# Performance work log

Hardware: AMD Instinct MI355X
Metric: run time of the kernel (lower is better)

## Reference

```python
import jax, jax.numpy as jnp
import numpy as np

N = 100000
E = 1000000
IN, HID, OUT = 128, 64, 40


def setup_inputs() -> dict:
    key = jax.random.key(0)
    k1, k2, k3, k4 = jax.random.split(key, 4)
    x = jax.random.normal(k1, (N, IN), dtype=jnp.float32)
    edge_index = jax.random.randint(k2, (2, E), 0, N, dtype=jnp.int64)
    W1 = jax.random.normal(k3, (IN, HID), dtype=jnp.float32) * (1.0 / np.sqrt(IN))
    b1 = jnp.zeros((HID,), dtype=jnp.float32)
    W2 = jax.random.normal(k4, (HID, OUT), dtype=jnp.float32) * (1.0 / np.sqrt(HID))
    b2 = jnp.zeros((OUT,), dtype=jnp.float32)
    return {"x": x, "edge_index": edge_index, "W1": W1, "b1": b1, "W2": W2, "b2": b2}


def _gcn_norm(edge_index, num_nodes):
    # PyG GCNConv default: add self-loops, symmetric normalization deg^-1/2 A deg^-1/2
    loop = jnp.arange(num_nodes, dtype=edge_index.dtype)
    src = jnp.concatenate([edge_index[0], loop])
    dst = jnp.concatenate([edge_index[1], loop])
    deg = jax.ops.segment_sum(jnp.ones_like(dst, dtype=jnp.float32), dst, num_segments=num_nodes)
    dinv = jnp.where(deg > 0, jax.lax.rsqrt(deg), 0.0)
    norm = dinv[src] * dinv[dst]  # [E+N]
    return src, dst, norm


def _gcn_conv(h, W, b, src, dst, norm, num_nodes):
    h = h @ W                          # [N, d_out] dense transform
    msg = h[src] * norm[:, None]       # gather + scale per edge
    out = jax.ops.segment_sum(msg, dst, num_segments=num_nodes)  # scatter-add
    return out + b


def reference(x, edge_index, W1, b1, W2, b2):
    src, dst, norm = _gcn_norm(edge_index, N)
    h = jax.nn.relu(_gcn_conv(x, W1, b1, src, dst, norm, N))
    # dropout is identity at inference (module in eval mode)
    out = _gcn_conv(h, W2, b2, src, dst, norm, N)
    return out
```

## Files before the change

### kernel.cpp

```cpp
#include <hip/hip_runtime.h>

#define NN 100000
#define EE 1000000
#define IN_F 128
#define HID_F 64
#define OUT_F 40
#define BUCKET 48
#define BIN_NODES 256
#define NBINS 391
#define FIFO_CAP 4096
#define P1_CHUNK 2048
#define P1_BUF 16

typedef _Float16 half8 __attribute__((ext_vector_type(8)));
typedef _Float16 half4 __attribute__((ext_vector_type(4)));
typedef float f32x4 __attribute__((ext_vector_type(4)));

#define SWZ(b, row) ((b) ^ (((row) & 7) << 4))

static __device__ __forceinline__ int atomic_add_i32(int* p, int v) {
    return __hip_atomic_fetch_add(p, v, __ATOMIC_RELAXED, __HIP_MEMORY_SCOPE_AGENT);
}

static __device__ __forceinline__ f32x4 h4f4(half4 h) {
    f32x4 r = {(float)h.x, (float)h.y, (float)h.z, (float)h.w};
    return r;
}

__global__ __launch_bounds__(256) void k_prep(const float* __restrict__ W1,
                                              const float* __restrict__ W2,
                                              _Float16* __restrict__ w1t,
                                              _Float16* __restrict__ w2t,
                                              int* __restrict__ bincur) {
    int i = blockIdx.x * 256 + threadIdx.x;
    if (i < IN_F * HID_F) {
        int k = i >> 6, n = i & 63;
        w1t[n * IN_F + k] = (_Float16)W1[i];
    }
    if (i < 48 * HID_F) {
        int n = i >> 6, k = i & 63;
        w2t[i] = (_Float16)((n < OUT_F) ? W2[k * OUT_F + n] : 0.f);
    }
    if (i < NBINS) bincur[i] = 0;
}

__global__ __launch_bounds__(256) void k_bin(const int* __restrict__ ei,
                                             int* __restrict__ bincur,
                                             unsigned* __restrict__ fifo) {
    __shared__ unsigned buf[NBINS][P1_BUF];
    __shared__ int lcnt[NBINS];
    __shared__ int lbase[NBINS];
    const int tid = threadIdx.x;
    for (int j = tid; j < NBINS; j += 256) lcnt[j] = 0;
    __syncthreads();

    const int e0 = blockIdx.x * P1_CHUNK;
    #pragma unroll
    for (int i = 0; i < P1_CHUNK / 256; ++i) {
        int e = e0 + i * 256 + tid;
        if (e < EE) {
            int s = ei[e];
            int d = ei[EE + e];
            int bin = d >> 8;
            unsigned pk = ((unsigned)s << 8) | (unsigned)(d & 255);
            int p = atomicAdd(&lcnt[bin], 1);
            if (p < P1_BUF) {
                buf[bin][p] = pk;
            } else {
                int gp = atomic_add_i32(&bincur[bin], 1);
                if (gp < FIFO_CAP) fifo[(size_t)bin * FIFO_CAP + gp] = pk;
            }
        }
    }
    __syncthreads();
    for (int j = tid; j < NBINS; j += 256) {
        int cnt = lcnt[j]; if (cnt > P1_BUF) cnt = P1_BUF;
        lbase[j] = (cnt > 0) ? atomic_add_i32(&bincur[j], cnt) : 0;
        lcnt[j] = cnt;
    }
    __syncthreads();
    for (int j = tid; j < NBINS; j += 256) {
        int cnt = lcnt[j];
        int base = lbase[j];
        for (int k = 0; k < cnt; ++k) {
            int gp = base + k;
            if (gp < FIFO_CAP) fifo[(size_t)j * FIFO_CAP + gp] = buf[j][k];
        }
    }
}

__global__ __launch_bounds__(256) void k_csr(const int* __restrict__ bincur,
                                             const unsigned* __restrict__ fifo,
                                             int* __restrict__ csr,
                                             int* __restrict__ deg,
                                             float* __restrict__ dinv) {
    __shared__ int cur[BIN_NODES];
    __shared__ int stage[BIN_NODES * BUCKET];
    const int tid = threadIdx.x;
    const int bin = blockIdx.x;
    const int v0 = bin * BIN_NODES;
    const int nnode = (NN - v0 < BIN_NODES) ? (NN - v0) : BIN_NODES;
    if (tid < BIN_NODES) cur[tid] = 0;
    __syncthreads();

    int cnt = bincur[bin]; if (cnt > FIFO_CAP) cnt = FIFO_CAP;
    for (int k = tid; k < cnt; k += 256) {
        unsigned u = fifo[(size_t)bin * FIFO_CAP + k];
        int dl = u & 255;
        int s = (int)(u >> 8);
        int p = atomicAdd(&cur[dl], 1);
        if (p < BUCKET) stage[dl * BUCKET + p] = s;
    }
    __syncthreads();

    if (tid < nnode) {
        int d = cur[tid]; if (d > BUCKET) d = BUCKET;
        int dpad = (d + 7) & ~7; if (dpad > BUCKET) dpad = BUCKET;
        for (int k = d; k < dpad; ++k) stage[tid * BUCKET + k] = NN;
        cur[tid] = d;
    }
    __syncthreads();

    const int total4 = nnode * BUCKET / 4;
    int4* dst4 = (int4*)&csr[(size_t)v0 * BUCKET];
    for (int idx = tid; idx < total4; idx += 256)
        dst4[idx] = *(const int4*)&stage[idx * 4];
    if (tid < nnode) {
        int d = cur[tid];
        deg[v0 + tid] = d;
        dinv[v0 + tid] = rsqrtf((float)(d + 1));
    }
}

__global__ __launch_bounds__(256) void k_gemm1(const float* __restrict__ x,
                                               const _Float16* __restrict__ w1t,
                                               const float* __restrict__ dinv,
                                               _Float16* __restrict__ h1s) {
    __shared__ _Float16 As[64 * IN_F];
    __shared__ _Float16 Bs[64 * IN_F];
    const int tid = threadIdx.x;
    const size_t r0 = (size_t)blockIdx.x * 64;

    #pragma unroll
    for (int i = 0; i < 8; ++i) {
        int f = i * 256 + tid;
        int row = f >> 5;
        int k4 = (f & 31) * 4;
        size_t gr = r0 + row; if (gr >= NN) gr = NN - 1;
        float4 v = *(const float4*)&x[gr * IN_F + k4];
        _Float16 h[4] = {(_Float16)v.x, (_Float16)v.y, (_Float16)v.z, (_Float16)v.w};
        *(uint2*)((char*)As + SWZ(row * 256 + k4 * 2, row)) = *(uint2*)h;
    }
    #pragma unroll
    for (int i = 0; i < 4; ++i) {
        int c = i * 256 + tid;
        int col = c >> 4;
        int k8 = (c & 15) * 8;
        uint4 v = *(const uint4*)&w1t[col * IN_F + k8];
        *(uint4*)((char*)Bs + SWZ(col * 256 + k8 * 2, col)) = v;
    }
    __syncthreads();

    const int w = tid >> 6, l = tid & 63;
    const int lr = l & 15, lg = l >> 4;
    const int R0 = w * 16;
    f32x4 acc[4] = {};
    #pragma unroll
    for (int kk = 0; kk < 4; ++kk) {
        const int kbyte = (kk * 32 + lg * 8) * 2;
        const int arow = R0 + lr;
        half8 a = *(const half8*)((const char*)As + SWZ(arow * 256 + kbyte, arow));
        #pragma unroll
        for (int t = 0; t < 4; ++t) {
            const int bcol = t * 16 + lr;
            half8 b = *(const half8*)((const char*)Bs + SWZ(bcol * 256 + kbyte, bcol));
            acc[t] = __builtin_amdgcn_mfma_f32_16x16x32_f16(a, b, acc[t], 0, 0, 0);
        }
    }
    #pragma unroll
    for (int r = 0; r < 4; ++r) {
        size_t row = r0 + R0 + lg * 4 + r;
        if (row < NN) {
            float dv = dinv[row];
            #pragma unroll
            for (int t = 0; t < 4; ++t)
                h1s[row * HID_F + t * 16 + lr] = (_Float16)(dv * acc[t][r]);
        } else if (row == NN) {
            #pragma unroll
            for (int t = 0; t < 4; ++t)
                h1s[row * HID_F + t * 16 + lr] = (_Float16)0.f;
        }
    }
}

__global__ __launch_bounds__(256) void k_agg1g2(const _Float16* __restrict__ h1s,
                                                const float* __restrict__ dinv,
                                                const int* __restrict__ degA,
                                                const int* __restrict__ csr,
                                                const float* __restrict__ b1,
                                                const _Float16* __restrict__ w2t,
                                                _Float16* __restrict__ tabA,
                                                _Float16* __restrict__ tabB) {
    __shared__ _Float16 As[64 * HID_F];
    __shared__ _Float16 Bs[48 * HID_F];
    const int tid = threadIdx.x;
    const size_t r0 = (size_t)blockIdx.x * 64;

    for (int cB = tid; cB < 384; cB += 256) {
        int col = cB >> 3;
        int k8 = (cB & 7) * 8;
        uint4 vB = *(const uint4*)&w2t[col * HID_F + k8];
        *(uint4*)((char*)Bs + SWZ(col * 128 + k8 * 2, col)) = vB;
    }

    const int grp = tid >> 4;
    const int c = tid & 15;
    float4 bb = *(const float4*)&b1[c * 4];
    #pragma unroll
    for (int i = 0; i < 4; ++i) {
        const int row = grp + i * 16;
        const size_t v = r0 + row;
        if (v >= NN) continue;

        int dg = degA[v];
        if (dg > BUCKET) dg = BUCKET;
        const int iters = (dg + 7) >> 3;
        const int4* cp = (const int4*)&csr[(size_t)v * BUCKET];

        f32x4 accA = h4f4(*(const half4*)&h1s[(v << 6) + c * 4]);
        f32x4 accB = {};
        for (int it = 0; it < iters; ++it) {
            int4 sa = cp[2 * it];
            int4 sb = cp[2 * it + 1];
            half4 a0 = *(const half4*)&h1s[((size_t)sa.x << 6) + c * 4];
            half4 a1 = *(const half4*)&h1s[((size_t)sa.y << 6) + c * 4];
            half4 a2 = *(const half4*)&h1s[((size_t)sa.z << 6) + c * 4];
            half4 a3 = *(const half4*)&h1s[((size_t)sa.w << 6) + c * 4];
            half4 a4 = *(const half4*)&h1s[((size_t)sb.x << 6) + c * 4];
            half4 a5 = *(const half4*)&h1s[((size_t)sb.y << 6) + c * 4];
            half4 a6 = *(const half4*)&h1s[((size_t)sb.z << 6) + c * 4];
            half4 a7 = *(const half4*)&h1s[((size_t)sb.w << 6) + c * 4];
            accA += h4f4(a0); accB += h4f4(a1); accA += h4f4(a2); accB += h4f4(a3);
            accA += h4f4(a4); accB += h4f4(a5); accA += h4f4(a6); accB += h4f4(a7);
        }
        accA += accB;

        const float dv = dinv[v];
        _Float16 o[4];
        o[0] = (_Float16)fmaxf(dv * accA[0] + bb.x, 0.f);
        o[1] = (_Float16)fmaxf(dv * accA[1] + bb.y, 0.f);
        o[2] = (_Float16)fmaxf(dv * accA[2] + bb.z, 0.f);
        o[3] = (_Float16)fmaxf(dv * accA[3] + bb.w, 0.f);
        *(uint2*)((char*)As + SWZ(row * 128 + c * 8, row)) = *(uint2*)o;
    }
    __syncthreads();

    const int w = tid >> 6, l = tid & 63;
    const int lr = l & 15, lg = l >> 4;
    const int R0 = w * 16;
    f32x4 acc[3] = {};
    #pragma unroll
    for (int kk = 0; kk < 2; ++kk) {
        const int kbyte = (kk * 32 + lg * 8) * 2;
        const int arow = R0 + lr;
        half8 a = *(const half8*)((const char*)As + SWZ(arow * 128 + kbyte, arow));
        #pragma unroll
        for (int t = 0; t < 3; ++t) {
            const int bcol = t * 16 + lr;
            half8 b = *(const half8*)((const char*)Bs + SWZ(bcol * 128 + kbyte, bcol));
            acc[t] = __builtin_amdgcn_mfma_f32_16x16x32_f16(a, b, acc[t], 0, 0, 0);
        }
    }
    #pragma unroll
    for (int r = 0; r < 4; ++r) {
        size_t row = r0 + R0 + lg * 4 + r;
        if (row < NN) {
            float dv = dinv[row];
            #pragma unroll
            for (int t = 0; t < 3; ++t) {
                int col = t * 16 + lr;
                float val = dv * acc[t][r];
                if (col < 32) tabA[row * 32 + col] = (_Float16)val;
                else if (col < OUT_F) tabB[row * 8 + (col - 32)] = (_Float16)val;
            }
        } else if (row == NN) {
            #pragma unroll
            for (int t = 0; t < 3; ++t) {
                int col = t * 16 + lr;
                if (col < 32) tabA[row * 32 + col] = (_Float16)0.f;
                else if (col < OUT_F) tabB[row * 8 + (col - 32)] = (_Float16)0.f;
            }
        }
    }
}

__global__ __launch_bounds__(256) void k_agg2(const _Float16* __restrict__ tabA,
                                              const _Float16* __restrict__ tabB,
                                              const float* __restrict__ dinv,
                                              const int* __restrict__ degA,
                                              const int* __restrict__ csr,
                                              const float* __restrict__ b2,
                                              float* __restrict__ out) {
    const int tid = threadIdx.x;
    const int v = blockIdx.x * 16 + (tid >> 4);
    if (v >= NN) return;
    const int c = tid & 15;
    const bool useA = (c < 8);
    const size_t aoff = useA ? (size_t)c * 4 : 0;
    const size_t boff = (c >= 8 && c < 10) ? (size_t)(c - 8) * 4 : 0;

    int dg = degA[v];
    if (dg > BUCKET) dg = BUCKET;
    const int iters = (dg + 7) >> 3;
    const int4* cp = (const int4*)&csr[(size_t)v * BUCKET];

    f32x4 accA, accB = {};
    {
        const _Float16* p = useA ? tabA + ((size_t)v << 5) + aoff : tabB + ((size_t)v << 3) + boff;
        accA = h4f4(*(const half4*)p);
    }
    for (int it = 0; it < iters; ++it) {
        int4 sa = cp[2 * it];
        int4 sb = cp[2 * it + 1];
        const _Float16* p0 = useA ? tabA + ((size_t)sa.x << 5) + aoff : tabB + ((size_t)sa.x << 3) + boff;
        const _Float16* p1 = useA ? tabA + ((size_t)sa.y << 5) + aoff : tabB + ((size_t)sa.y << 3) + boff;
        const _Float16* p2 = useA ? tabA + ((size_t)sa.z << 5) + aoff : tabB + ((size_t)sa.z << 3) + boff;
        const _Float16* p3 = useA ? tabA + ((size_t)sa.w << 5) + aoff : tabB + ((size_t)sa.w << 3) + boff;
        const _Float16* p4 = useA ? tabA + ((size_t)sb.x << 5) + aoff : tabB + ((size_t)sb.x << 3) + boff;
        const _Float16* p5 = useA ? tabA + ((size_t)sb.y << 5) + aoff : tabB + ((size_t)sb.y << 3) + boff;
        const _Float16* p6 = useA ? tabA + ((size_t)sb.z << 5) + aoff : tabB + ((size_t)sb.z << 3) + boff;
        const _Float16* p7 = useA ? tabA + ((size_t)sb.w << 5) + aoff : tabB + ((size_t)sb.w << 3) + boff;
        half4 a0 = *(const half4*)p0;
        half4 a1 = *(const half4*)p1;
        half4 a2 = *(const half4*)p2;
        half4 a3 = *(const half4*)p3;
        half4 a4 = *(const half4*)p4;
        half4 a5 = *(const half4*)p5;
        half4 a6 = *(const half4*)p6;
        half4 a7 = *(const half4*)p7;
        accA += h4f4(a0); accB += h4f4(a1); accA += h4f4(a2); accB += h4f4(a3);
        accA += h4f4(a4); accB += h4f4(a5); accA += h4f4(a6); accB += h4f4(a7);
    }
    accA += accB;

    if (c < 10) {
        const float dv = dinv[v];
        float4 bb = *(const float4*)&b2[c * 4];
        float4 o = {dv * accA[0] + bb.x, dv * accA[1] + bb.y,
                    dv * accA[2] + bb.z, dv * accA[3] + bb.w};
        *(float4*)&out[(size_t)v * OUT_F + c * 4] = o;
    }
}

extern "C" void kernel_launch(void* const* d_in, const int* in_sizes, int n_in,
                              void* d_out, int out_size, void* d_ws, size_t ws_size,
                              hipStream_t stream) {
    const float* x  = (const float*)d_in[0];
    const int*   ei = (const int*)d_in[1];
    const float* W1 = (const float*)d_in[2];
    const float* b1 = (const float*)d_in[3];
    const float* W2 = (const float*)d_in[4];
    const float* b2 = (const float*)d_in[5];
    float* out = (float*)d_out;

    char* p = (char*)d_ws;
    float*     dinv   = (float*)p;     p += (size_t)NN * 4;
    int*       deg    = (int*)p;       p += (size_t)NN * 4;
    int*       bincur = (int*)p;       p += 512 * 4;
    unsigned*  fifo   = (unsigned*)p;  p += (size_t)NBINS * FIFO_CAP * 4;
    _Float16*  w1t    = (_Float16*)p;  p += (size_t)IN_F * HID_F * 2;
    _Float16*  w2t    = (_Float16*)p;  p += (size_t)48 * HID_F * 2;
    int*       csr    = (int*)p;       p += (size_t)NN * BUCKET * 4;
    _Float16*  h1s    = (_Float16*)p;  p += (size_t)(NN + 1) * HID_F * 2;
    _Float16*  tabA   = (_Float16*)p;  p += (size_t)(NN + 1) * 32 * 2;
    _Float16*  tabB   = (_Float16*)p;  p += ((size_t)(NN + 1) * 8 + 32) * 2;

    const int gemm_blocks = (NN + 63) / 64;
    const int agg2_blocks = (NN + 15) / 16;
    const int bin_blocks = (EE + P1_CHUNK - 1) / P1_CHUNK;

    k_prep  <<<32, 256, 0, stream>>>(W1, W2, w1t, w2t, bincur);
    k_bin   <<<bin_blocks, 256, 0, stream>>>(ei, bincur, fifo);
    k_csr   <<<NBINS, 256, 0, stream>>>(bincur, fifo, csr, deg, dinv);
    k_gemm1 <<<gemm_blocks, 256, 0, stream>>>(x, w1t, dinv, h1s);
    k_agg1g2<<<gemm_blocks, 256, 0, stream>>>(h1s, dinv, deg, csr, b1, w2t, tabA, tabB);
    k_agg2  <<<agg2_blocks, 256, 0, stream>>>(tabA, tabB, dinv, deg, csr, b2, out);
}
```

Before: 106.2 us.

## Merge edge binning with first GEMM in one launch; apply source dinv during aggregation

The edge-binning pass and the dense X·W1 transform now run as separate block ranges of a single kernel, so the two independent stages can overlap on the GPU. To make that possible, the GEMM no longer scales rows by dinv, because dinv is only computed later in the CSR kernel. The aggregation kernel therefore gathers dinv per source edge, and each block converts W1 and W2 to fp16 itself instead of using a prep kernel. The bincur reset becomes a memset. The cost is an extra dinv gather per edge in aggregation and a slower, strided W1 transpose repeated in every GEMM block.

```diff
diff --git a/kernel.cpp b/kernel.cpp
--- a/kernel.cpp
+++ b/kernel.cpp
@@ -11,6 +11,8 @@
 #define FIFO_CAP 4096
 #define P1_CHUNK 2048
 #define P1_BUF 16
+#define BIN_BLOCKS ((EE + P1_CHUNK - 1) / P1_CHUNK)
+#define GEMM_BLOCKS ((NN + 63) / 64)
 
 typedef _Float16 half8 __attribute__((ext_vector_type(8)));
 typedef _Float16 half4 __attribute__((ext_vector_type(4)));
@@ -27,64 +29,105 @@
     return r;
 }
 
-__global__ __launch_bounds__(256) void k_prep(const float* __restrict__ W1,
-                                              const float* __restrict__ W2,
-                                              _Float16* __restrict__ w1t,
-                                              _Float16* __restrict__ w2t,
-                                              int* __restrict__ bincur) {
-    int i = blockIdx.x * 256 + threadIdx.x;
-    if (i < IN_F * HID_F) {
-        int k = i >> 6, n = i & 63;
-        w1t[n * IN_F + k] = (_Float16)W1[i];
-    }
-    if (i < 48 * HID_F) {
-        int n = i >> 6, k = i & 63;
-        w2t[i] = (_Float16)((n < OUT_F) ? W2[k * OUT_F + n] : 0.f);
-    }
-    if (i < NBINS) bincur[i] = 0;
-}
-
-__global__ __launch_bounds__(256) void k_bin(const int* __restrict__ ei,
+__global__ __launch_bounds__(256) void k_fat(const int* __restrict__ ei,
                                              int* __restrict__ bincur,
-                                             unsigned* __restrict__ fifo) {
-    __shared__ unsigned buf[NBINS][P1_BUF];
-    __shared__ int lcnt[NBINS];
-    __shared__ int lbase[NBINS];
+                                             unsigned* __restrict__ fifo,
+                                             const float* __restrict__ x,
+                                             const float* __restrict__ W1,
+                                             _Float16* __restrict__ h1) {
+    __shared__ __align__(16) char smem[32768];
     const int tid = threadIdx.x;
-    for (int j = tid; j < NBINS; j += 256) lcnt[j] = 0;
-    __syncthreads();
-
-    const int e0 = blockIdx.x * P1_CHUNK;
-    #pragma unroll
-    for (int i = 0; i < P1_CHUNK / 256; ++i) {
-        int e = e0 + i * 256 + tid;
-        if (e < EE) {
-            int s = ei[e];
-            int d = ei[EE + e];
-            int bin = d >> 8;
-            unsigned pk = ((unsigned)s << 8) | (unsigned)(d & 255);
-            int p = atomicAdd(&lcnt[bin], 1);
-            if (p < P1_BUF) {
-                buf[bin][p] = pk;
-            } else {
-                int gp = atomic_add_i32(&bincur[bin], 1);
-                if (gp < FIFO_CAP) fifo[(size_t)bin * FIFO_CAP + gp] = pk;
-            }
-        }
-    }
-    __syncthreads();
-    for (int j = tid; j < NBINS; j += 256) {
-        int cnt = lcnt[j]; if (cnt > P1_BUF) cnt = P1_BUF;
-        lbase[j] = (cnt > 0) ? atomic_add_i32(&bincur[j], cnt) : 0;
-        lcnt[j] = cnt;
-    }
-    __syncthreads();
-    for (int j = tid; j < NBINS; j += 256) {
-        int cnt = lcnt[j];
-        int base = lbase[j];
-        for (int k = 0; k < cnt; ++k) {
-            int gp = base + k;
-            if (gp < FIFO_CAP) fifo[(size_t)j * FIFO_CAP + gp] = buf[j][k];
+
+    if (blockIdx.x < BIN_BLOCKS) {
+        unsigned (*buf)[P1_BUF] = (unsigned (*)[P1_BUF])smem;
+        int* lcnt  = (int*)(smem + 25024);
+        int* lbase = (int*)(smem + 25024 + 1600);
+        for (int j = tid; j < NBINS; j += 256) lcnt[j] = 0;
+        __syncthreads();
+
+        const int e0 = blockIdx.x * P1_CHUNK;
+        #pragma unroll
+        for (int i = 0; i < P1_CHUNK / 256; ++i) {
+            int e = e0 + i * 256 + tid;
+            if (e < EE) {
+                int s = ei[e];
+                int d = ei[EE + e];
+                int bin = d >> 8;
+                unsigned pk = ((unsigned)s << 8) | (unsigned)(d & 255);
+                int p = atomicAdd(&lcnt[bin], 1);
+                if (p < P1_BUF) {
+                    buf[bin][p] = pk;
+                } else {
+                    int gp = atomic_add_i32(&bincur[bin], 1);
+                    if (gp < FIFO_CAP) fifo[(size_t)bin * FIFO_CAP + gp] = pk;
+                }
+            }
+        }
+        __syncthreads();
+        for (int j = tid; j < NBINS; j += 256) {
+            int cnt = lcnt[j]; if (cnt > P1_BUF) cnt = P1_BUF;
+            lbase[j] = (cnt > 0) ? atomic_add_i32(&bincur[j], cnt) : 0;
+            lcnt[j] = cnt;
+        }
+        __syncthreads();
+        for (int j = tid; j < NBINS; j += 256) {
+            int cnt = lcnt[j];
+            int base = lbase[j];
+            for (int k = 0; k < cnt; ++k) {
+                int gp = base + k;
+                if (gp < FIFO_CAP) fifo[(size_t)j * FIFO_CAP + gp] = buf[j][k];
+            }
+        }
+    } else {
+        _Float16* As = (_Float16*)smem;
+        _Float16* Bs = (_Float16*)(smem + 16384);
+        const size_t r0 = (size_t)(blockIdx.x - BIN_BLOCKS) * 64;
+
+        #pragma unroll
+        for (int i = 0; i < 8; ++i) {
+            int f = i * 256 + tid;
+            int row = f >> 5;
+            int k4 = (f & 31) * 4;
+            size_t gr = r0 + row; if (gr >= NN) gr = NN - 1;
+            float4 v = *(const float4*)&x[gr * IN_F + k4];
+            _Float16 h[4] = {(_Float16)v.x, (_Float16)v.y, (_Float16)v.z, (_Float16)v.w};
+            *(uint2*)((char*)As + SWZ(row * 256 + k4 * 2, row)) = *(uint2*)h;
+        }
+        for (int i = tid; i < IN_F * HID_F; i += 256) {
+            int col = i >> 7, k = i & 127;
+            _Float16 w = (_Float16)W1[k * HID_F + col];
+            *(_Float16*)((char*)Bs + SWZ(col * 256 + k * 2, col)) = w;
+        }
+        __syncthreads();
+
+        const int w = tid >> 6, l = tid & 63;
+        const int lr = l & 15, lg = l >> 4;
+        const int R0 = w * 16;
+        f32x4 acc[4] = {};
+        #pragma unroll
+        for (int kk = 0; kk < 4; ++kk) {
+            const int kbyte = (kk * 32 + lg * 8) * 2;
+            const int arow = R0 + lr;
+            half8 a = *(const half8*)((const char*)As + SWZ(arow * 256 + kbyte, arow));
+            #pragma unroll
+            for (int t = 0; t < 4; ++t) {
+                const int bcol = t * 16 + lr;
+                half8 b = *(const half8*)((const char*)Bs + SWZ(bcol * 256 + kbyte, bcol));
+                acc[t] = __builtin_amdgcn_mfma_f32_16x16x32_f16(a, b, acc[t], 0, 0, 0);
+            }
+        }
+        #pragma unroll
+        for (int r = 0; r < 4; ++r) {
+            size_t row = r0 + R0 + lg * 4 + r;
+            if (row < NN) {
+                #pragma unroll
+                for (int t = 0; t < 4; ++t)
+                    h1[row * HID_F + t * 16 + lr] = (_Float16)acc[t][r];
+            } else if (row == NN) {
+                #pragma unroll
+                for (int t = 0; t < 4; ++t)
+                    h1[row * HID_F + t * 16 + lr] = (_Float16)0.f;
+            }
         }
     }
 }
@@ -130,75 +173,15 @@
         deg[v0 + tid] = d;
         dinv[v0 + tid] = rsqrtf((float)(d + 1));
     }
-}
-
-__global__ __launch_bounds__(256) void k_gemm1(const float* __restrict__ x,
-                                               const _Float16* __restrict__ w1t,
-                                               const float* __restrict__ dinv,
-                                               _Float16* __restrict__ h1s) {
-    __shared__ _Float16 As[64 * IN_F];
-    __shared__ _Float16 Bs[64 * IN_F];
-    const int tid = threadIdx.x;
-    const size_t r0 = (size_t)blockIdx.x * 64;
-
-    #pragma unroll
-    for (int i = 0; i < 8; ++i) {
-        int f = i * 256 + tid;
-        int row = f >> 5;
-        int k4 = (f & 31) * 4;
-        size_t gr = r0 + row; if (gr >= NN) gr = NN - 1;
-        float4 v = *(const float4*)&x[gr * IN_F + k4];
-        _Float16 h[4] = {(_Float16)v.x, (_Float16)v.y, (_Float16)v.z, (_Float16)v.w};
-        *(uint2*)((char*)As + SWZ(row * 256 + k4 * 2, row)) = *(uint2*)h;
-    }
-    #pragma unroll
-    for (int i = 0; i < 4; ++i) {
-        int c = i * 256 + tid;
-        int col = c >> 4;
-        int k8 = (c & 15) * 8;
-        uint4 v = *(const uint4*)&w1t[col * IN_F + k8];
-        *(uint4*)((char*)Bs + SWZ(col * 256 + k8 * 2, col)) = v;
-    }
-    __syncthreads();
-
-    const int w = tid >> 6, l = tid & 63;
-    const int lr = l & 15, lg = l >> 4;
-    const int R0 = w * 16;
-    f32x4 acc[4] = {};
-    #pragma unroll
-    for (int kk = 0; kk < 4; ++kk) {
-        const int kbyte = (kk * 32 + lg * 8) * 2;
-        const int arow = R0 + lr;
-        half8 a = *(const half8*)((const char*)As + SWZ(arow * 256 + kbyte, arow));
-        #pragma unroll
-        for (int t = 0; t < 4; ++t) {
-            const int bcol = t * 16 + lr;
-            half8 b = *(const half8*)((const char*)Bs + SWZ(bcol * 256 + kbyte, bcol));
-            acc[t] = __builtin_amdgcn_mfma_f32_16x16x32_f16(a, b, acc[t], 0, 0, 0);
-        }
-    }
-    #pragma unroll
-    for (int r = 0; r < 4; ++r) {
-        size_t row = r0 + R0 + lg * 4 + r;
-        if (row < NN) {
-            float dv = dinv[row];
-            #pragma unroll
-            for (int t = 0; t < 4; ++t)
-                h1s[row * HID_F + t * 16 + lr] = (_Float16)(dv * acc[t][r]);
-        } else if (row == NN) {
-            #pragma unroll
-            for (int t = 0; t < 4; ++t)
-                h1s[row * HID_F + t * 16 + lr] = (_Float16)0.f;
-        }
-    }
-}
-
-__global__ __launch_bounds__(256) void k_agg1g2(const _Float16* __restrict__ h1s,
+    if (bin == 0 && tid == 0) dinv[NN] = 0.f;
+}
+
+__global__ __launch_bounds__(256) void k_agg1g2(const _Float16* __restrict__ h1,
                                                 const float* __restrict__ dinv,
                                                 const int* __restrict__ degA,
                                                 const int* __restrict__ csr,
                                                 const float* __restrict__ b1,
-                                                const _Float16* __restrict__ w2t,
+                                                const float* __restrict__ W2,
                                                 _Float16* __restrict__ tabA,
                                                 _Float16* __restrict__ tabB) {
     __shared__ _Float16 As[64 * HID_F];
@@ -206,11 +189,10 @@
     const int tid = threadIdx.x;
     const size_t r0 = (size_t)blockIdx.x * 64;
 
-    for (int cB = tid; cB < 384; cB += 256) {
-        int col = cB >> 3;
-        int k8 = (cB & 7) * 8;
-        uint4 vB = *(const uint4*)&w2t[col * HID_F + k8];
-        *(uint4*)((char*)Bs + SWZ(col * 128 + k8 * 2, col)) = vB;
+    for (int i = tid; i < 48 * HID_F; i += 256) {
+        int col = i >> 6, k = i & 63;
+        _Float16 w = (_Float16)((col < OUT_F) ? W2[k * OUT_F + col] : 0.f);
+        *(_Float16*)((char*)Bs + SWZ(col * 128 + k * 2, col)) = w;
     }
 
     const int grp = tid >> 4;
@@ -227,30 +209,34 @@
         const int iters = (dg + 7) >> 3;
         const int4* cp = (const int4*)&csr[(size_t)v * BUCKET];
 
-        f32x4 accA = h4f4(*(const half4*)&h1s[(v << 6) + c * 4]);
+        const float dvv = dinv[v];
+        f32x4 accA = dvv * h4f4(*(const half4*)&h1[(v << 6) + c * 4]);
         f32x4 accB = {};
         for (int it = 0; it < iters; ++it) {
             int4 sa = cp[2 * it];
             int4 sb = cp[2 * it + 1];
-            half4 a0 = *(const half4*)&h1s[((size_t)sa.x << 6) + c * 4];
-            half4 a1 = *(const half4*)&h1s[((size_t)sa.y << 6) + c * 4];
-            half4 a2 = *(const half4*)&h1s[((size_t)sa.z << 6) + c * 4];
-            half4 a3 = *(const half4*)&h1s[((size_t)sa.w << 6) + c * 4];
-            half4 a4 = *(const half4*)&h1s[((size_t)sb.x << 6) + c * 4];
-            half4 a5 = *(const half4*)&h1s[((size_t)sb.y << 6) + c * 4];
-            half4 a6 = *(const half4*)&h1s[((size_t)sb.z << 6) + c * 4];
-            half4 a7 = *(const half4*)&h1s[((size_t)sb.w << 6) + c * 4];
-            accA += h4f4(a0); accB += h4f4(a1); accA += h4f4(a2); accB += h4f4(a3);
-            accA += h4f4(a4); accB += h4f4(a5); accA += h4f4(a6); accB += h4f4(a7);
+            float d0 = dinv[sa.x], d1 = dinv[sa.y], d2 = dinv[sa.z], d3 = dinv[sa.w];
+            float d4 = dinv[sb.x], d5 = dinv[sb.y], d6 = dinv[sb.z], d7 = dinv[sb.w];
+            half4 a0 = *(const half4*)&h1[((size_t)sa.x << 6) + c * 4];
+            half4 a1 = *(const half4*)&h1[((size_t)sa.y << 6) + c * 4];
+            half4 a2 = *(const half4*)&h1[((size_t)sa.z << 6) + c * 4];
+            half4 a3 = *(const half4*)&h1[((size_t)sa.w << 6) + c * 4];
+            half4 a4 = *(const half4*)&h1[((size_t)sb.x << 6) + c * 4];
+            half4 a5 = *(const half4*)&h1[((size_t)sb.y << 6) + c * 4];
+            half4 a6 = *(const half4*)&h1[((size_t)sb.z << 6) + c * 4];
+            half4 a7 = *(const half4*)&h1[((size_t)sb.w << 6) + c * 4];
+            accA += d0 * h4f4(a0); accB += d1 * h4f4(a1);
+            accA += d2 * h4f4(a2); accB += d3 * h4f4(a3);
+            accA += d4 * h4f4(a4); accB += d5 * h4f4(a5);
+            accA += d6 * h4f4(a6); accB += d7 * h4f4(a7);
         }
         accA += accB;
 
-        const float dv = dinv[v];
         _Float16 o[4];
-        o[0] = (_Float16)fmaxf(dv * accA[0] + bb.x, 0.f);
-        o[1] = (_Float16)fmaxf(dv * accA[1] + bb.y, 0.f);
-        o[2] = (_Float16)fmaxf(dv * accA[2] + bb.z, 0.f);
-        o[3] = (_Float16)fmaxf(dv * accA[3] + bb.w, 0.f);
+        o[0] = (_Float16)fmaxf(dvv * accA[0] + bb.x, 0.f);
+        o[1] = (_Float16)fmaxf(dvv * accA[1] + bb.y, 0.f);
+        o[2] = (_Float16)fmaxf(dvv * accA[2] + bb.z, 0.f);
+        o[3] = (_Float16)fmaxf(dvv * accA[3] + bb.w, 0.f);
         *(uint2*)((char*)As + SWZ(row * 128 + c * 8, row)) = *(uint2*)o;
     }
     __syncthreads();
@@ -364,25 +350,20 @@
     float* out = (float*)d_out;
 
     char* p = (char*)d_ws;
-    float*     dinv   = (float*)p;     p += (size_t)NN * 4;
+    float*     dinv   = (float*)p;     p += (size_t)(NN + 1) * 4;
     int*       deg    = (int*)p;       p += (size_t)NN * 4;
     int*       bincur = (int*)p;       p += 512 * 4;
     unsigned*  fifo   = (unsigned*)p;  p += (size_t)NBINS * FIFO_CAP * 4;
-    _Float16*  w1t    = (_Float16*)p;  p += (size_t)IN_F * HID_F * 2;
-    _Float16*  w2t    = (_Float16*)p;  p += (size_t)48 * HID_F * 2;
     int*       csr    = (int*)p;       p += (size_t)NN * BUCKET * 4;
-    _Float16*  h1s    = (_Float16*)p;  p += (size_t)(NN + 1) * HID_F * 2;
+    _Float16*  h1     = (_Float16*)p;  p += (size_t)(NN + 1) * HID_F * 2;
     _Float16*  tabA   = (_Float16*)p;  p += (size_t)(NN + 1) * 32 * 2;
     _Float16*  tabB   = (_Float16*)p;  p += ((size_t)(NN + 1) * 8 + 32) * 2;
 
-    const int gemm_blocks = (NN + 63) / 64;
     const int agg2_blocks = (NN + 15) / 16;
-    const int bin_blocks = (EE + P1_CHUNK - 1) / P1_CHUNK;
-
-    k_prep  <<<32, 256, 0, stream>>>(W1, W2, w1t, w2t, bincur);
-    k_bin   <<<bin_blocks, 256, 0, stream>>>(ei, bincur, fifo);
+
+    hipMemsetAsync(bincur, 0, 512 * 4, stream);
+    k_fat   <<<BIN_BLOCKS + GEMM_BLOCKS, 256, 0, stream>>>(ei, bincur, fifo, x, W1, h1);
     k_csr   <<<NBINS, 256, 0, stream>>>(bincur, fifo, csr, deg, dinv);
-    k_gemm1 <<<gemm_blocks, 256, 0, stream>>>(x, w1t, dinv, h1s);
-    k_agg1g2<<<gemm_blocks, 256, 0, stream>>>(h1s, dinv, deg, csr, b1, w2t, tabA, tabB);
+    k_agg1g2<<<GEMM_BLOCKS, 256, 0, stream>>>(h1, dinv, deg, csr, b1, W2, tabA, tabB);
     k_agg2  <<<agg2_blocks, 256, 0, stream>>>(tabA, tabB, dinv, deg, csr, b2, out);
 }
```

Result: slower. 159.9 us (+50.6%).

## Replace global bin FIFO atomics with per-block fixed segments plus small overflow

Applied to the files above, without the earlier changes.

The edge binning pass now writes each block's per-bin local buffer into a fixed, private segment indexed by (bin, block), with a per-segment count, and drops the per-bin global atomic reservation. Only edges that overflow the 16-entry local buffer go through a global atomic into a small per-bin overflow FIFO. The CSR builder walks each bin's per-block segments and then the overflow list. This removes global atomic contention in the binning pass, but the CSR kernel now reads segments serially per thread, and the overflow capacity of 64 per bin may silently drop edges if a block's local buffer overflows often.

```diff
diff --git a/kernel.cpp b/kernel.cpp
--- a/kernel.cpp
+++ b/kernel.cpp
@@ -8,9 +8,10 @@
 #define BUCKET 48
 #define BIN_NODES 256
 #define NBINS 391
-#define FIFO_CAP 4096
 #define P1_CHUNK 2048
 #define P1_BUF 16
+#define BIN_BLOCKS ((EE + P1_CHUNK - 1) / P1_CHUNK)
+#define OV_CAP 64
 
 typedef _Float16 half8 __attribute__((ext_vector_type(8)));
 typedef _Float16 half4 __attribute__((ext_vector_type(4)));
@@ -31,7 +32,7 @@
                                               const float* __restrict__ W2,
                                               _Float16* __restrict__ w1t,
                                               _Float16* __restrict__ w2t,
-                                              int* __restrict__ bincur) {
+                                              int* __restrict__ ocnt) {
     int i = blockIdx.x * 256 + threadIdx.x;
     if (i < IN_F * HID_F) {
         int k = i >> 6, n = i & 63;
@@ -41,20 +42,22 @@
         int n = i >> 6, k = i & 63;
         w2t[i] = (_Float16)((n < OUT_F) ? W2[k * OUT_F + n] : 0.f);
     }
-    if (i < NBINS) bincur[i] = 0;
+    if (i < NBINS) ocnt[i] = 0;
 }
 
 __global__ __launch_bounds__(256) void k_bin(const int* __restrict__ ei,
-                                             int* __restrict__ bincur,
-                                             unsigned* __restrict__ fifo) {
+                                             int* __restrict__ ocnt,
+                                             unsigned* __restrict__ ofifo,
+                                             int* __restrict__ lcnt2,
+                                             unsigned* __restrict__ fifo2) {
     __shared__ unsigned buf[NBINS][P1_BUF];
     __shared__ int lcnt[NBINS];
-    __shared__ int lbase[NBINS];
-    const int tid = threadIdx.x;
+    const int tid = threadIdx.x;
+    const int b = blockIdx.x;
     for (int j = tid; j < NBINS; j += 256) lcnt[j] = 0;
     __syncthreads();
 
-    const int e0 = blockIdx.x * P1_CHUNK;
+    const int e0 = b * P1_CHUNK;
     #pragma unroll
     for (int i = 0; i < P1_CHUNK / 256; ++i) {
         int e = e0 + i * 256 + tid;
@@ -67,30 +70,24 @@
             if (p < P1_BUF) {
                 buf[bin][p] = pk;
             } else {
-                int gp = atomic_add_i32(&bincur[bin], 1);
-                if (gp < FIFO_CAP) fifo[(size_t)bin * FIFO_CAP + gp] = pk;
+                int gp = atomic_add_i32(&ocnt[bin], 1);
+                if (gp < OV_CAP) ofifo[bin * OV_CAP + gp] = pk;
             }
         }
     }
     __syncthreads();
     for (int j = tid; j < NBINS; j += 256) {
         int cnt = lcnt[j]; if (cnt > P1_BUF) cnt = P1_BUF;
-        lbase[j] = (cnt > 0) ? atomic_add_i32(&bincur[j], cnt) : 0;
-        lcnt[j] = cnt;
-    }
-    __syncthreads();
-    for (int j = tid; j < NBINS; j += 256) {
-        int cnt = lcnt[j];
-        int base = lbase[j];
-        for (int k = 0; k < cnt; ++k) {
-            int gp = base + k;
-            if (gp < FIFO_CAP) fifo[(size_t)j * FIFO_CAP + gp] = buf[j][k];
-        }
-    }
-}
-
-__global__ __launch_bounds__(256) void k_csr(const int* __restrict__ bincur,
-                                             const unsigned* __restrict__ fifo,
+        lcnt2[j * BIN_BLOCKS + b] = cnt;
+        unsigned* seg = &fifo2[((size_t)j * BIN_BLOCKS + b) * P1_BUF];
+        for (int k = 0; k < cnt; ++k) seg[k] = buf[j][k];
+    }
+}
+
+__global__ __launch_bounds__(256) void k_csr(const int* __restrict__ lcnt2,
+                                             const unsigned* __restrict__ fifo2,
+                                             const int* __restrict__ ocnt,
+                                             const unsigned* __restrict__ ofifo,
                                              int* __restrict__ csr,
                                              int* __restrict__ deg,
                                              float* __restrict__ dinv) {
@@ -103,13 +100,26 @@
     if (tid < BIN_NODES) cur[tid] = 0;
     __syncthreads();
 
-    int cnt = bincur[bin]; if (cnt > FIFO_CAP) cnt = FIFO_CAP;
-    for (int k = tid; k < cnt; k += 256) {
-        unsigned u = fifo[(size_t)bin * FIFO_CAP + k];
-        int dl = u & 255;
-        int s = (int)(u >> 8);
-        int p = atomicAdd(&cur[dl], 1);
-        if (p < BUCKET) stage[dl * BUCKET + p] = s;
+    for (int blk = tid; blk < BIN_BLOCKS; blk += 256) {
+        int cnt = lcnt2[bin * BIN_BLOCKS + blk];
+        const unsigned* seg = &fifo2[((size_t)bin * BIN_BLOCKS + blk) * P1_BUF];
+        for (int k = 0; k < cnt; ++k) {
+            unsigned u = seg[k];
+            int dl = u & 255;
+            int s = (int)(u >> 8);
+            int p = atomicAdd(&cur[dl], 1);
+            if (p < BUCKET) stage[dl * BUCKET + p] = s;
+        }
+    }
+    {
+        int oc = ocnt[bin]; if (oc > OV_CAP) oc = OV_CAP;
+        for (int k = tid; k < oc; k += 256) {
+            unsigned u = ofifo[bin * OV_CAP + k];
+            int dl = u & 255;
+            int s = (int)(u >> 8);
+            int p = atomicAdd(&cur[dl], 1);
+            if (p < BUCKET) stage[dl * BUCKET + p] = s;
+        }
     }
     __syncthreads();
 
@@ -366,8 +376,10 @@
     char* p = (char*)d_ws;
     float*     dinv   = (float*)p;     p += (size_t)NN * 4;
     int*       deg    = (int*)p;       p += (size_t)NN * 4;
-    int*       bincur = (int*)p;       p += 512 * 4;
-    unsigned*  fifo   = (unsigned*)p;  p += (size_t)NBINS * FIFO_CAP * 4;
+    int*       ocnt   = (int*)p;       p += 512 * 4;
+    unsigned*  ofifo  = (unsigned*)p;  p += (size_t)NBINS * OV_CAP * 4;
+    int*       lcnt2  = (int*)p;       p += (size_t)NBINS * BIN_BLOCKS * 4;
+    unsigned*  fifo2  = (unsigned*)p;  p += (size_t)NBINS * BIN_BLOCKS * P1_BUF * 4;
     _Float16*  w1t    = (_Float16*)p;  p += (size_t)IN_F * HID_F * 2;
     _Float16*  w2t    = (_Float16*)p;  p += (size_t)48 * HID_F * 2;
     int*       csr    = (int*)p;       p += (size_t)NN * BUCKET * 4;
@@ -377,11 +389,10 @@
 
     const int gemm_blocks = (NN + 63) / 64;
     const int agg2_blocks = (NN + 15) / 16;
-    const int bin_blocks = (EE + P1_CHUNK - 1) / P1_CHUNK;
-
-    k_prep  <<<32, 256, 0, stream>>>(W1, W2, w1t, w2t, bincur);
-    k_bin   <<<bin_blocks, 256, 0, stream>>>(ei, bincur, fifo);
-    k_csr   <<<NBINS, 256, 0, stream>>>(bincur, fifo, csr, deg, dinv);
+
+    k_prep  <<<32, 256, 0, stream>>>(W1, W2, w1t, w2t, ocnt);
+    k_bin   <<<BIN_BLOCKS, 256, 0, stream>>>(ei, ocnt, ofifo, lcnt2, fifo2);
+    k_csr   <<<NBINS, 256, 0, stream>>>(lcnt2, fifo2, ocnt, ofifo, csr, deg, dinv);
     k_gemm1 <<<gemm_blocks, 256, 0, stream>>>(x, w1t, dinv, h1s);
     k_agg1g2<<<gemm_blocks, 256, 0, stream>>>(h1s, dinv, deg, csr, b1, w2t, tabA, tabB);
     k_agg2  <<<agg2_blocks, 256, 0, stream>>>(tabA, tabB, dinv, deg, csr, b2, out);
```

New measurement: 116.7 us. 1.1x slower.

## Slice feature tables into 16-column planes for cache-local gather aggregation

Applied to the files above, without the earlier changes.

Stores the hidden and output feature tables as separate 16-column planes (32 bytes per node). Block indices are interleaved so that concurrently running blocks work on the same plane and its working set can stay in L2/MALL during the random neighbor gathers. This splits the fused aggregate+GEMM2 kernel into a separate aggregation kernel and a GEMM2 kernel, which adds a kernel launch and a round trip of the ReLU activations through global memory. The output gather is also padded to 48 columns across three planes.

```diff
diff --git a/kernel.cpp b/kernel.cpp
--- a/kernel.cpp
+++ b/kernel.cpp
@@ -11,6 +11,7 @@
 #define FIFO_CAP 4096
 #define P1_CHUNK 2048
 #define P1_BUF 16
+#define NWORK 1563
 
 typedef _Float16 half8 __attribute__((ext_vector_type(8)));
 typedef _Float16 half4 __attribute__((ext_vector_type(4)));
@@ -135,7 +136,7 @@
 __global__ __launch_bounds__(256) void k_gemm1(const float* __restrict__ x,
                                                const _Float16* __restrict__ w1t,
                                                const float* __restrict__ dinv,
-                                               _Float16* __restrict__ h1s) {
+                                               _Float16* __restrict__ h1sl) {
     __shared__ _Float16 As[64 * IN_F];
     __shared__ _Float16 Bs[64 * IN_F];
     const int tid = threadIdx.x;
@@ -184,74 +185,88 @@
             float dv = dinv[row];
             #pragma unroll
             for (int t = 0; t < 4; ++t)
-                h1s[row * HID_F + t * 16 + lr] = (_Float16)(dv * acc[t][r]);
+                h1sl[((size_t)t * (NN + 1) + row) * 16 + lr] = (_Float16)(dv * acc[t][r]);
         } else if (row == NN) {
             #pragma unroll
             for (int t = 0; t < 4; ++t)
-                h1s[row * HID_F + t * 16 + lr] = (_Float16)0.f;
-        }
-    }
-}
-
-__global__ __launch_bounds__(256) void k_agg1g2(const _Float16* __restrict__ h1s,
+                h1sl[((size_t)t * (NN + 1) + row) * 16 + lr] = (_Float16)0.f;
+        }
+    }
+}
+
+__global__ __launch_bounds__(256) void k_agg1sl(const _Float16* __restrict__ h1sl,
                                                 const float* __restrict__ dinv,
-                                                const int* __restrict__ degA,
+                                                const int* __restrict__ deg,
                                                 const int* __restrict__ csr,
                                                 const float* __restrict__ b1,
-                                                const _Float16* __restrict__ w2t,
-                                                _Float16* __restrict__ tabA,
-                                                _Float16* __restrict__ tabB) {
+                                                _Float16* __restrict__ hrelusl) {
+    const int b = blockIdx.x;
+    const int s = (b & 7) >> 1;
+    const int w = ((b >> 3) << 1) | (b & 1);
+    if (w >= NWORK) return;
+    const int tid = threadIdx.x;
+    const int v = w * 64 + (tid >> 2);
+    if (v >= NN) return;
+    const int c = tid & 3;
+
+    const _Float16* tab = h1sl + (size_t)s * (NN + 1) * 16;
+    int dg = deg[v];
+    if (dg > BUCKET) dg = BUCKET;
+    const int iters = (dg + 7) >> 3;
+    const int4* cp = (const int4*)&csr[(size_t)v * BUCKET];
+
+    f32x4 accA = h4f4(*(const half4*)&tab[(size_t)v * 16 + c * 4]);
+    f32x4 accB = {};
+    for (int it = 0; it < iters; ++it) {
+        int4 sa = cp[2 * it];
+        int4 sb = cp[2 * it + 1];
+        half4 a0 = *(const half4*)&tab[(size_t)sa.x * 16 + c * 4];
+        half4 a1 = *(const half4*)&tab[(size_t)sa.y * 16 + c * 4];
+        half4 a2 = *(const half4*)&tab[(size_t)sa.z * 16 + c * 4];
+        half4 a3 = *(const half4*)&tab[(size_t)sa.w * 16 + c * 4];
+        half4 a4 = *(const half4*)&tab[(size_t)sb.x * 16 + c * 4];
+        half4 a5 = *(const half4*)&tab[(size_t)sb.y * 16 + c * 4];
+        half4 a6 = *(const half4*)&tab[(size_t)sb.z * 16 + c * 4];
+        half4 a7 = *(const half4*)&tab[(size_t)sb.w * 16 + c * 4];
+        accA += h4f4(a0); accB += h4f4(a1); accA += h4f4(a2); accB += h4f4(a3);
+        accA += h4f4(a4); accB += h4f4(a5); accA += h4f4(a6); accB += h4f4(a7);
+    }
+    accA += accB;
+
+    const float dv = dinv[v];
+    float4 bb = *(const float4*)&b1[s * 16 + c * 4];
+    _Float16 o[4];
+    o[0] = (_Float16)fmaxf(dv * accA[0] + bb.x, 0.f);
+    o[1] = (_Float16)fmaxf(dv * accA[1] + bb.y, 0.f);
+    o[2] = (_Float16)fmaxf(dv * accA[2] + bb.z, 0.f);
+    o[3] = (_Float16)fmaxf(dv * accA[3] + bb.w, 0.f);
+    *(uint2*)&hrelusl[((size_t)s * (NN + 1) + v) * 16 + c * 4] = *(uint2*)o;
+}
+
+__global__ __launch_bounds__(256) void k_gemm2(const _Float16* __restrict__ hrelusl,
+                                               const _Float16* __restrict__ w2t,
+                                               const float* __restrict__ dinv,
+                                               _Float16* __restrict__ tabsl) {
     __shared__ _Float16 As[64 * HID_F];
     __shared__ _Float16 Bs[48 * HID_F];
     const int tid = threadIdx.x;
     const size_t r0 = (size_t)blockIdx.x * 64;
 
+    #pragma unroll
+    for (int i = 0; i < 2; ++i) {
+        int cI = i * 256 + tid;
+        int row = cI >> 3;
+        int sc = cI & 7;
+        size_t gr = r0 + row; if (gr >= NN) gr = NN - 1;
+        const _Float16* src = hrelusl + ((size_t)(sc >> 1) * (NN + 1) + gr) * 16 + (sc & 1) * 8;
+        uint4 v = *(const uint4*)src;
+        *(uint4*)((char*)As + SWZ(row * 128 + sc * 16, row)) = v;
+    }
     for (int cB = tid; cB < 384; cB += 256) {
         int col = cB >> 3;
         int k8 = (cB & 7) * 8;
         uint4 vB = *(const uint4*)&w2t[col * HID_F + k8];
         *(uint4*)((char*)Bs + SWZ(col * 128 + k8 * 2, col)) = vB;
-    }
-
-    const int grp = tid >> 4;
-    const int c = tid & 15;
-    float4 bb = *(const float4*)&b1[c * 4];
-    #pragma unroll
-    for (int i = 0; i < 4; ++i) {
-        const int row = grp + i * 16;
-        const size_t v = r0 + row;
-        if (v >= NN) continue;
-
-        int dg = degA[v];
-        if (dg > BUCKET) dg = BUCKET;
-        const int iters = (dg + 7) >> 3;
-        const int4* cp = (const int4*)&csr[(size_t)v * BUCKET];
-
-        f32x4 accA = h4f4(*(const half4*)&h1s[(v << 6) + c * 4]);
-        f32x4 accB = {};
-        for (int it = 0; it < iters; ++it) {
-            int4 sa = cp[2 * it];
-            int4 sb = cp[2 * it + 1];
-            half4 a0 = *(const half4*)&h1s[((size_t)sa.x << 6) + c * 4];
-            half4 a1 = *(const half4*)&h1s[((size_t)sa.y << 6) + c * 4];
-            half4 a2 = *(const half4*)&h1s[((size_t)sa.z << 6) + c * 4];
-            half4 a3 = *(const half4*)&h1s[((size_t)sa.w << 6) + c * 4];
-            half4 a4 = *(const half4*)&h1s[((size_t)sb.x << 6) + c * 4];
-            half4 a5 = *(const half4*)&h1s[((size_t)sb.y << 6) + c * 4];
-            half4 a6 = *(const half4*)&h1s[((size_t)sb.z << 6) + c * 4];
-            half4 a7 = *(const half4*)&h1s[((size_t)sb.w << 6) + c * 4];
-            accA += h4f4(a0); accB += h4f4(a1); accA += h4f4(a2); accB += h4f4(a3);
-            accA += h4f4(a4); accB += h4f4(a5); accA += h4f4(a6); accB += h4f4(a7);
-        }
-        accA += accB;
-
-        const float dv = dinv[v];
-        _Float16 o[4];
-        o[0] = (_Float16)fmaxf(dv * accA[0] + bb.x, 0.f);
-        o[1] = (_Float16)fmaxf(dv * accA[1] + bb.y, 0.f);
-        o[2] = (_Float16)fmaxf(dv * accA[2] + bb.z, 0.f);
-        o[3] = (_Float16)fmaxf(dv * accA[3] + bb.w, 0.f);
-        *(uint2*)((char*)As + SWZ(row * 128 + c * 8, row)) = *(uint2*)o;
     }
     __syncthreads();
 
@@ -279,76 +294,68 @@
             #pragma unroll
             for (int t = 0; t < 3; ++t) {
                 int col = t * 16 + lr;
-                float val = dv * acc[t][r];
-                if (col < 32) tabA[row * 32 + col] = (_Float16)val;
-                else if (col < OUT_F) tabB[row * 8 + (col - 32)] = (_Float16)val;
+                float val = (col < OUT_F) ? dv * acc[t][r] : 0.f;
+                tabsl[((size_t)t * (NN + 1) + row) * 16 + lr] = (_Float16)val;
             }
         } else if (row == NN) {
             #pragma unroll
-            for (int t = 0; t < 3; ++t) {
-                int col = t * 16 + lr;
-                if (col < 32) tabA[row * 32 + col] = (_Float16)0.f;
-                else if (col < OUT_F) tabB[row * 8 + (col - 32)] = (_Float16)0.f;
-            }
-        }
-    }
-}
-
-__global__ __launch_bounds__(256) void k_agg2(const _Float16* __restrict__ tabA,
-                                              const _Float16* __restrict__ tabB,
-                                              const float* __restrict__ dinv,
-                                              const int* __restrict__ degA,
-                                              const int* __restrict__ csr,
-                                              const float* __restrict__ b2,
-                                              float* __restrict__ out) {
-    const int tid = threadIdx.x;
-    const int v = blockIdx.x * 16 + (tid >> 4);
+            for (int t = 0; t < 3; ++t)
+                tabsl[((size_t)t * (NN + 1) + row) * 16 + lr] = (_Float16)0.f;
+        }
+    }
+}
+
+__global__ __launch_bounds__(256) void k_agg2sl(const _Float16* __restrict__ tabsl,
+                                                const float* __restrict__ dinv,
+                                                const int* __restrict__ deg,
+                                                const int* __restrict__ csr,
+                                                const float* __restrict__ b2,
+                                                float* __restrict__ out) {
+    const int b = blockIdx.x;
+    const int m = b & 7;
+    int s, i3, per;
+    if (m < 3)      { s = 0; i3 = m;     per = 3; }
+    else if (m < 6) { s = 1; i3 = m - 3; per = 3; }
+    else            { s = 2; i3 = m - 6; per = 2; }
+    const int w = (b >> 3) * per + i3;
+    if (w >= NWORK) return;
+    const int tid = threadIdx.x;
+    const int c = tid & 3;
+    if (s == 2 && c >= 2) return;
+    const int v = w * 64 + (tid >> 2);
     if (v >= NN) return;
-    const int c = tid & 15;
-    const bool useA = (c < 8);
-    const size_t aoff = useA ? (size_t)c * 4 : 0;
-    const size_t boff = (c >= 8 && c < 10) ? (size_t)(c - 8) * 4 : 0;
-
-    int dg = degA[v];
+
+    const _Float16* tab = tabsl + (size_t)s * (NN + 1) * 16;
+    int dg = deg[v];
     if (dg > BUCKET) dg = BUCKET;
     const int iters = (dg + 7) >> 3;
     const int4* cp = (const int4*)&csr[(size_t)v * BUCKET];
 
-    f32x4 accA, accB = {};
-    {
-        const _Float16* p = useA ? tabA + ((size_t)v << 5) + aoff : tabB + ((size_t)v << 3) + boff;
-        accA = h4f4(*(const half4*)p);
-    }
+    f32x4 accA = h4f4(*(const half4*)&tab[(size_t)v * 16 + c * 4]);
+    f32x4 accB = {};
     for (int it = 0; it < iters; ++it) {
         int4 sa = cp[2 * it];
         int4 sb = cp[2 * it + 1];
-        const _Float16* p0 = useA ? tabA + ((size_t)sa.x << 5) + aoff : tabB + ((size_t)sa.x << 3) + boff;
-        const _Float16* p1 = useA ? tabA + ((size_t)sa.y << 5) + aoff : tabB + ((size_t)sa.y << 3) + boff;
-        const _Float16* p2 = useA ? tabA + ((size_t)sa.z << 5) + aoff : tabB + ((size_t)sa.z << 3) + boff;
-        const _Float16* p3 = useA ? tabA + ((size_t)sa.w << 5) + aoff : tabB + ((size_t)sa.w << 3) + boff;
-        const _Float16* p4 = useA ? tabA + ((size_t)sb.x << 5) + aoff : tabB + ((size_t)sb.x << 3) + boff;
-        const _Float16* p5 = useA ? tabA + ((size_t)sb.y << 5) + aoff : tabB + ((size_t)sb.y << 3) + boff;
-        const _Float16* p6 = useA ? tabA + ((size_t)sb.z << 5) + aoff : tabB + ((size_t)sb.z << 3) + boff;
-        const _Float16* p7 = useA ? tabA + ((size_t)sb.w << 5) + aoff : tabB + ((size_t)sb.w << 3) + boff;
-        half4 a0 = *(const half4*)p0;
-        half4 a1 = *(const half4*)p1;
-        half4 a2 = *(const half4*)p2;
-        half4 a3 = *(const half4*)p3;
-        half4 a4 = *(const half4*)p4;
-        half4 a5 = *(const half4*)p5;
-        half4 a6 = *(const half4*)p6;
-        half4 a7 = *(const half4*)p7;
+        half4 a0 = *(const half4*)&tab[(size_t)sa.x * 16 + c * 4];
+        half4 a1 = *(const half4*)&tab[(size_t)sa.y * 16 + c * 4];
+        half4 a2 = *(const half4*)&tab[(size_t)sa.z * 16 + c * 4];
+        half4 a3 = *(const half4*)&tab[(size_t)sa.w * 16 + c * 4];
+        half4 a4 = *(const half4*)&tab[(size_t)sb.x * 16 + c * 4];
+        half4 a5 = *(const half4*)&tab[(size_t)sb.y * 16 + c * 4];
+        half4 a6 = *(const half4*)&tab[(size_t)sb.z * 16 + c * 4];
+        half4 a7 = *(const half4*)&tab[(size_t)sb.w * 16 + c * 4];
         accA += h4f4(a0); accB += h4f4(a1); accA += h4f4(a2); accB += h4f4(a3);
         accA += h4f4(a4); accB += h4f4(a5); accA += h4f4(a6); accB += h4f4(a7);
     }
     accA += accB;
 
-    if (c < 10) {
+    const int col0 = s * 16 + c * 4;
+    if (col0 < OUT_F) {
         const float dv = dinv[v];
-        float4 bb = *(const float4*)&b2[c * 4];
+        float4 bb = *(const float4*)&b2[col0];
         float4 o = {dv * accA[0] + bb.x, dv * accA[1] + bb.y,
                     dv * accA[2] + bb.z, dv * accA[3] + bb.w};
-        *(float4*)&out[(size_t)v * OUT_F + c * 4] = o;
+        *(float4*)&out[(size_t)v * OUT_F + col0] = o;
     }
 }
 
@@ -364,25 +371,26 @@
     float* out = (float*)d_out;
 
     char* p = (char*)d_ws;
-    float*     dinv   = (float*)p;     p += (size_t)NN * 4;
-    int*       deg    = (int*)p;       p += (size_t)NN * 4;
-    int*       bincur = (int*)p;       p += 512 * 4;
-    unsigned*  fifo   = (unsigned*)p;  p += (size_t)NBINS * FIFO_CAP * 4;
-    _Float16*  w1t    = (_Float16*)p;  p += (size_t)IN_F * HID_F * 2;
-    _Float16*  w2t    = (_Float16*)p;  p += (size_t)48 * HID_F * 2;
-    int*       csr    = (int*)p;       p += (size_t)NN * BUCKET * 4;
-    _Float16*  h1s    = (_Float16*)p;  p += (size_t)(NN + 1) * HID_F * 2;
-    _Float16*  tabA   = (_Float16*)p;  p += (size_t)(NN + 1) * 32 * 2;
-    _Float16*  tabB   = (_Float16*)p;  p += ((size_t)(NN + 1) * 8 + 32) * 2;
-
-    const int gemm_blocks = (NN + 63) / 64;
-    const int agg2_blocks = (NN + 15) / 16;
+    float*     dinv    = (float*)p;     p += (size_t)NN * 4;
+    int*       deg     = (int*)p;       p += (size_t)NN * 4;
+    int*       bincur  = (int*)p;       p += 512 * 4;
+    unsigned*  fifo    = (unsigned*)p;  p += (size_t)NBINS * FIFO_CAP * 4;
+    _Float16*  w1t     = (_Float16*)p;  p += (size_t)IN_F * HID_F * 2;
+    _Float16*  w2t     = (_Float16*)p;  p += (size_t)48 * HID_F * 2;
+    int*       csr     = (int*)p;       p += (size_t)NN * BUCKET * 4;
+    _Float16*  h1sl    = (_Float16*)p;  p += (size_t)4 * (NN + 1) * 16 * 2;
+    _Float16*  hrelusl = (_Float16*)p;  p += (size_t)4 * (NN + 1) * 16 * 2;
+    _Float16*  tabsl   = (_Float16*)p;  p += (size_t)3 * (NN + 1) * 16 * 2;
+
+    const int gemm_blocks = NWORK;
     const int bin_blocks = (EE + P1_CHUNK - 1) / P1_CHUNK;
+    const int sl_blocks = ((NWORK + 1) / 2) * 8;
 
     k_prep  <<<32, 256, 0, stream>>>(W1, W2, w1t, w2t, bincur);
     k_bin   <<<bin_blocks, 256, 0, stream>>>(ei, bincur, fifo);
     k_csr   <<<NBINS, 256, 0, stream>>>(bincur, fifo, csr, deg, dinv);
-    k_gemm1 <<<gemm_blocks, 256, 0, stream>>>(x, w1t, dinv, h1s);
-    k_agg1g2<<<gemm_blocks, 256, 0, stream>>>(h1s, dinv, deg, csr, b1, w2t, tabA, tabB);
-    k_agg2  <<<agg2_blocks, 256, 0, stream>>>(tabA, tabB, dinv, deg, csr, b2, out);
-}
+    k_gemm1 <<<gemm_blocks, 256, 0, stream>>>(x, w1t, dinv, h1sl);
+    k_agg1sl<<<sl_blocks, 256, 0, stream>>>(h1sl, dinv, deg, csr, b1, hrelusl);
+    k_gemm2 <<<gemm_blocks, 256, 0, stream>>>(hrelusl, w2t, dinv, tabsl);
+    k_agg2sl<<<sl_blocks, 256, 0, stream>>>(tabsl, dinv, deg, csr, b2, out);
+}
```

Measured after the change: 127.8 us. +20.3%, slower.
